# Kernel optimization log

Hardware: AMD Instinct MI355X
Metric: run time of the kernel (lower is better)

## Reference

```python
import jax, jax.numpy as jnp
import numpy as np

NUM_EMBEDDINGS = 256
EMBEDDING_DIM = 8


def setup_inputs() -> dict:
    key = jax.random.key(0)
    ks = jax.random.split(key, 8)
    B, D_in, H, D_out = 1024, 512, 2048, 512
    s = lambda fan: 1.0 / np.sqrt(fan)
    return {
        "x": jax.random.normal(ks[0], (B, D_in), dtype=jnp.float32),
        "emb_W": jax.random.normal(ks[1], (NUM_EMBEDDINGS, EMBEDDING_DIM), dtype=jnp.float32),
        "W_in": jax.random.normal(ks[2], (H, D_in), dtype=jnp.float32) * s(D_in),
        "b_in": jax.random.normal(ks[3], (H,), dtype=jnp.float32) * s(D_in),
        "W_h": jax.random.normal(ks[4], (H, H), dtype=jnp.float32) * s(H),
        "b_h": jax.random.normal(ks[5], (H,), dtype=jnp.float32) * s(H),
        "W_out": jax.random.normal(ks[6], (D_out, H), dtype=jnp.float32) * s(H),
        "b_out": jax.random.normal(ks[7], (D_out,), dtype=jnp.float32) * s(H),
    }


def reference(x, emb_W, W_in, b_in, W_h, b_h, W_out, b_out):
    B, D_in = x.shape
    flat = x.reshape(-1)  # [B*D_in], row-major flatten == torch .flatten()
    # power-feature expansion: powers 1..embedding_dim stacked on axis 1
    exps = jnp.arange(1, EMBEDDING_DIM + 1, dtype=x.dtype)
    x_res = flat[:, None] ** exps[None, :]  # [B*D_in, E]
    # get_ind: NOTE source uses sum(flat_x) (not sum of squares) -- faithful
    sm = jnp.sum(x_res, axis=1, keepdims=True)              # [N,1]
    emb = jnp.sum(emb_W * emb_W, axis=1)[None, :]           # [1,K]
    dist = sm + emb - 2.0 * (x_res @ emb_W.T)               # [N,K]
    ind = jnp.argmin(dist, axis=1)                          # [N] int
    # q = ind.view_as(x.T).T : reshape to [D_in, B] then transpose
    q = ind.reshape(D_in, B).T.astype(x.dtype)              # [B, D_in]
    # straight-through: forward value q, gradient flows to x
    q = x + jax.lax.stop_gradient(q - x)
    relu = jax.nn.relu
    h = relu(q @ W_in.T + b_in)      # d_in
    for _ in range(4):               # shared d_h applied 4 times
        h = relu(h @ W_h.T + b_h)
    f = relu(h @ W_out.T + b_out)    # d_out
    q_latent_loss = jnp.float32(0.0)  # eval mode
    return (f, q_latent_loss)
```

## Files before the change

### kernel.cpp

```cpp
#include <hip/hip_runtime.h>
#include <hip/hip_bf16.h>
#include <math.h>


#define B_ROWS 1024
#define D_IN   512
#define HDIM   2048
#define NTOT   (B_ROWS * D_IN)
#define NCODE  256
#define EDIM   8

typedef __attribute__((ext_vector_type(8))) short bf16x8;
typedef __attribute__((ext_vector_type(4))) float f32x4;

__device__ inline void gload_lds16(const void* g, void* l) {
    __builtin_amdgcn_global_load_lds(
        (const __attribute__((address_space(1))) void*)g,
        (__attribute__((address_space(3))) void*)l, 16, 0, 0);
}

__device__ inline ushort bf16_hi_bits(float v, float* hi_f) {
    __hip_bfloat16 h = __float2bfloat16(v);
    *hi_f = __bfloat162float(h);
    ushort u; __builtin_memcpy(&u, &h, 2); return u;
}
__device__ inline ushort bf16_bits(float v) {
    __hip_bfloat16 h = __float2bfloat16(v);
    ushort u; __builtin_memcpy(&u, &h, 2); return u;
}

__global__ __launch_bounds__(256) void fused_pre(
    const float* __restrict__ x, const float* __restrict__ embW,
    const float* __restrict__ Wi, const float* __restrict__ Wh,
    ushort* __restrict__ qhi,
    ushort* __restrict__ wihi, ushort* __restrict__ wilo,
    ushort* __restrict__ whhi, ushort* __restrict__ whlo,
    float* __restrict__ loss_out)
{
    __shared__ float sWE[NCODE][12];
    const int tid = threadIdx.x;

    if (blockIdx.x >= 1024) {
        const int sidx = blockIdx.x - 1024;
        #pragma unroll
        for (int s = 0; s < 4; ++s) {
            const int g = sidx * 1024 + s * 256 + tid;
            const float* src; ushort* hi; ushort* lo; int j;
            if (g < 262144) { src = Wi; hi = wihi; lo = wilo; j = g; }
            else            { src = Wh; hi = whhi; lo = whlo; j = g - 262144; }
            float4 v = reinterpret_cast<const float4*>(src)[j];
            float f[4] = {v.x, v.y, v.z, v.w};
            ushort hh[4], ll[4];
            #pragma unroll
            for (int c = 0; c < 4; ++c) {
                float hf;
                hh[c] = bf16_hi_bits(f[c], &hf);
                ll[c] = bf16_bits(f[c] - hf);
            }
            ushort4 h4 = {hh[0], hh[1], hh[2], hh[3]};
            ushort4 l4 = {ll[0], ll[1], ll[2], ll[3]};
            reinterpret_cast<ushort4*>(hi)[j] = h4;
            reinterpret_cast<ushort4*>(lo)[j] = l4;
        }
        return;
    }

    {
        const float4 a4 = *reinterpret_cast<const float4*>(&embW[tid * EDIM]);
        const float4 b4 = *reinterpret_cast<const float4*>(&embW[tid * EDIM + 4]);
        float s0 = __fmul_rn(a4.x, a4.x), s1 = __fmul_rn(a4.y, a4.y);
        float s2 = __fmul_rn(a4.z, a4.z), s3 = __fmul_rn(a4.w, a4.w);
        float s4 = __fmul_rn(b4.x, b4.x), s5 = __fmul_rn(b4.y, b4.y);
        float s6 = __fmul_rn(b4.z, b4.z), s7 = __fmul_rn(b4.w, b4.w);
        float a = __fadd_rn(__fadd_rn(s0, s1), __fadd_rn(s2, s3));
        float b = __fadd_rn(__fadd_rn(s4, s5), __fadd_rn(s6, s7));
        sWE[tid][0] = a4.x; sWE[tid][1] = a4.y; sWE[tid][2] = a4.z; sWE[tid][3] = a4.w;
        sWE[tid][4] = b4.x; sWE[tid][5] = b4.y; sWE[tid][6] = b4.z; sWE[tid][7] = b4.w;
        sWE[tid][8] = __fadd_rn(a, b);
    }
    __syncthreads();

    const int nbase = blockIdx.x * 512 + tid;

    float p2[2][EDIM], sm[2];
    #pragma unroll
    for (int j = 0; j < 2; ++j) {
        const float v = x[nbase + j * 256];
        float p[EDIM];
        #pragma unroll
        for (int e = 0; e < EDIM; ++e)
            p[e] = powf(v, (float)(e + 1));
        float a = __fadd_rn(__fadd_rn(p[0], p[1]), __fadd_rn(p[2], p[3]));
        float b = __fadd_rn(__fadd_rn(p[4], p[5]), __fadd_rn(p[6], p[7]));
        sm[j] = __fadd_rn(a, b);
        #pragma unroll
        for (int e = 0; e < EDIM; ++e)
            p2[j][e] = 2.0f * p[e];
    }

    float best[2] = {INFINITY, INFINITY};
    int   bi[2]   = {0, 0};
    for (int k = 0; k < NCODE; ++k) {
        const float4 w0 = *reinterpret_cast<const float4*>(&sWE[k][0]);
        const float4 w1 = *reinterpret_cast<const float4*>(&sWE[k][4]);
        const float  Ek = sWE[k][8];
        #pragma unroll
        for (int j = 0; j < 2; ++j) {
            float dot = 0.f;
            dot = fmaf(p2[j][0], w0.x, dot); dot = fmaf(p2[j][1], w0.y, dot);
            dot = fmaf(p2[j][2], w0.z, dot); dot = fmaf(p2[j][3], w0.w, dot);
            dot = fmaf(p2[j][4], w1.x, dot); dot = fmaf(p2[j][5], w1.y, dot);
            dot = fmaf(p2[j][6], w1.z, dot); dot = fmaf(p2[j][7], w1.w, dot);
            float d = __fsub_rn(__fadd_rn(sm[j], Ek), dot);
            if (d < best[j]) { best[j] = d; bi[j] = k; }
        }
    }

    #pragma unroll
    for (int j = 0; j < 2; ++j) {
        const int n  = nbase + j * 256;
        const int bo = n & (B_ROWS - 1);
        const int dd = n >> 10;
        qhi[bo * D_IN + dd] = bf16_bits((float)bi[j]);
    }
    if (blockIdx.x == 0 && tid == 0) loss_out[0] = 0.0f;
}

__global__ __launch_bounds__(256) void wo_split(
    const float* __restrict__ Wo, ushort* __restrict__ hi, ushort* __restrict__ lo)
{
    const int tid = threadIdx.x;
    #pragma unroll
    for (int s = 0; s < 4; ++s) {
        const int j = blockIdx.x * 1024 + s * 256 + tid;
        float4 v = reinterpret_cast<const float4*>(Wo)[j];
        float f[4] = {v.x, v.y, v.z, v.w};
        ushort hh[4], ll[4];
        #pragma unroll
        for (int c = 0; c < 4; ++c) {
            float hf;
            hh[c] = bf16_hi_bits(f[c], &hf);
            ll[c] = bf16_bits(f[c] - hf);
        }
        ushort4 h4 = {hh[0], hh[1], hh[2], hh[3]};
        ushort4 l4 = {ll[0], ll[1], ll[2], ll[3]};
        reinterpret_cast<ushort4*>(hi)[j] = h4;
        reinterpret_cast<ushort4*>(lo)[j] = l4;
    }
}

template<bool ALO, bool PARTIAL>
__global__ __launch_bounds__(256) void gemm_split(
    const ushort* __restrict__ Ahi, const ushort* __restrict__ Alo,
    const ushort* __restrict__ Whi, const ushort* __restrict__ Wlo,
    const float* __restrict__ bias,
    ushort* __restrict__ Ohi, ushort* __restrict__ Olo,
    float* __restrict__ OF, int N, int K, int klen)
{
    constexpr int BUF = 49152;
    constexpr int OFF_AH = 0, OFF_AL = 8192, OFF_BH = 16384;
    __shared__ char lds[2 * BUF];

    const int tid = threadIdx.x, lane = tid & 63, wid = tid >> 6;

    const int gy = gridDim.y;
    const int nwg = gridDim.x * gy;
    int lin = blockIdx.x * gy + blockIdx.y;
    int q   = nwg >> 3;
    int sw  = (lin & 7) * q + (lin >> 3);
    int bx  = sw / gy, by2 = sw % gy;
    const int bm   = (by2 & 15) << 6;
    const int kz   = by2 >> 4;
    const int kbeg = kz * klen;
    const int bn   = bx << 7;

    const int wm = (wid >> 1) << 5;
    const int wn = (wid & 1) << 6;

    constexpr int NSEGW = ALO ? 12 : 10;
    const ushort* gp[NSEGW];
    uint ldsoff[NSEGW];
    #pragma unroll
    for (int i = 0; i < NSEGW; ++i) {
        int s = wid + i * 4;
        const ushort* pl; int row0, base, sip;
        if (ALO) {
            if (s < 8)       { pl = Ahi; row0 = bm; base = OFF_AH;         sip = s; }
            else if (s < 16) { pl = Alo; row0 = bm; base = OFF_AL;         sip = s - 8; }
            else if (s < 32) { pl = Whi; row0 = bn; base = OFF_BH;         sip = s - 16; }
            else             { pl = Wlo; row0 = bn; base = OFF_BH + 16384; sip = s - 32; }
        } else {
            if (s < 8)       { pl = Ahi; row0 = bm; base = OFF_AH;         sip = s; }
            else if (s < 24) { pl = Whi; row0 = bn; base = OFF_BH;         sip = s - 8; }
            else             { pl = Wlo; row0 = bn; base = OFF_BH + 16384; sip = s - 24; }
        }
        int r  = sip * 8 + (lane >> 3);
        int ch = (lane & 7) ^ (r & 7);
        gp[i]     = pl + (size_t)(row0 + r) * K + kbeg + ch * 8;
        ldsoff[i] = base + sip * 1024;
    }

    uint aoff[2][2], boff[4][2];
    #pragma unroll
    for (int f = 0; f < 2; ++f) {
        int ar = wm + f * 16 + (lane & 15);
        #pragma unroll
        for (int s = 0; s < 2; ++s) {
            int ch = (s * 4 + (lane >> 4)) ^ (ar & 7);
            aoff[f][s] = OFF_AH + ar * 128 + ch * 16;
        }
    }
    #pragma unroll
    for (int f = 0; f < 4; ++f) {
        int br = wn + f * 16 + (lane & 15);
        #pragma unroll
        for (int s = 0; s < 2; ++s) {
            int ch = (s * 4 + (lane >> 4)) ^ (br & 7);
            boff[f][s] = OFF_BH + br * 128 + ch * 16;
        }
    }

    auto stage = [&](int kt, int b) {
        #pragma unroll
        for (int i = 0; i < NSEGW; ++i)
            gload_lds16(gp[i] + kt * 64, lds + b * BUF + ldsoff[i]);
    };

    f32x4 acc[2][4] = {};
    const int NT = klen >> 6;

    stage(0, 0);
    __syncthreads();

    for (int t = 0; t < NT; ++t) {
        const int cur = t & 1;
        if (t + 1 < NT) stage(t + 1, cur ^ 1);

        const char* lb = lds + cur * BUF;
        bf16x8 aH[2][2], aL[2][2], bH[2][4], bL[2][4];
        #pragma unroll
        for (int s = 0; s < 2; ++s) {
            #pragma unroll
            for (int f = 0; f < 2; ++f) {
                aH[s][f] = *(const bf16x8*)(lb + aoff[f][s]);
                if constexpr (ALO) aL[s][f] = *(const bf16x8*)(lb + aoff[f][s] + 8192);
            }
            #pragma unroll
            for (int f = 0; f < 4; ++f) {
                bH[s][f] = *(const bf16x8*)(lb + boff[f][s]);
                bL[s][f] = *(const bf16x8*)(lb + boff[f][s] + 16384);
            }
        }
        #pragma unroll
        for (int s = 0; s < 2; ++s) {
            #pragma unroll
            for (int fm = 0; fm < 2; ++fm)
                #pragma unroll
                for (int fn = 0; fn < 4; ++fn)
                    acc[fm][fn] = __builtin_amdgcn_mfma_f32_16x16x32_bf16(
                        aH[s][fm], bH[s][fn], acc[fm][fn], 0, 0, 0);
            #pragma unroll
            for (int fm = 0; fm < 2; ++fm)
                #pragma unroll
                for (int fn = 0; fn < 4; ++fn)
                    acc[fm][fn] = __builtin_amdgcn_mfma_f32_16x16x32_bf16(
                        aH[s][fm], bL[s][fn], acc[fm][fn], 0, 0, 0);
            if constexpr (ALO) {
                #pragma unroll
                for (int fm = 0; fm < 2; ++fm)
                    #pragma unroll
                    for (int fn = 0; fn < 4; ++fn)
                        acc[fm][fn] = __builtin_amdgcn_mfma_f32_16x16x32_bf16(
                            aL[s][fm], bH[s][fn], acc[fm][fn], 0, 0, 0);
            }
        }
        __syncthreads();
    }

    #pragma unroll
    for (int fm = 0; fm < 2; ++fm) {
        #pragma unroll
        for (int fn = 0; fn < 4; ++fn) {
            const int col = bn + wn + fn * 16 + (lane & 15);
            const int rb  = bm + wm + fm * 16 + ((lane >> 4) << 2);
            if constexpr (PARTIAL) {
                #pragma unroll
                for (int r = 0; r < 4; ++r)
                    OF[(size_t)(kz * B_ROWS + rb + r) * N + col] = acc[fm][fn][r];
            } else {
                const float bc = bias[col];
                #pragma unroll
                for (int r = 0; r < 4; ++r) {
                    float v = acc[fm][fn][r] + bc;
                    v = v > 0.f ? v : 0.f;
                    float hf;
                    ushort hb = bf16_hi_bits(v, &hf);
                    Ohi[(size_t)(rb + r) * N + col] = hb;
                    Olo[(size_t)(rb + r) * N + col] = bf16_bits(v - hf);
                }
            }
        }
    }
}

__global__ __launch_bounds__(256) void gemm_mid(
    const ushort* __restrict__ Ahi, const ushort* __restrict__ Alo,
    const ushort* __restrict__ Bhi, const ushort* __restrict__ Blo,
    float* __restrict__ OF, int N, int Kfull, int klen)
{
    constexpr int BUF = 65536;
    constexpr int OFF_A[2] = {0, 16384};
    constexpr int OFF_B[2] = {32768, 49152};
    __shared__ char lds[2 * BUF];

    const int tid = threadIdx.x, lane = tid & 63, wid = tid >> 6;

    const int gy = gridDim.y;
    const int nwg = gridDim.x * gy;
    int lin = blockIdx.x * gy + blockIdx.y;
    int q   = nwg >> 3;
    int sw  = (lin & 7) * q + (lin >> 3);
    int bx  = sw / gy, by2 = sw % gy;
    const int bm   = (by2 & 7) << 7;
    const int kz   = by2 >> 3;
    const int kbeg = kz * klen;
    const int bn   = bx << 7;

    const int wm = (wid >> 1) << 6;
    const int wn = (wid & 1) << 6;

    const int ch0 = (lane & 7) ^ (lane >> 3);
    const size_t kstep8 = (size_t)Kfull * 8;
    const ushort* gpb[4];
    uint lob[4];
    {
        const ushort* pls[4] = {Ahi, Alo, Bhi, Blo};
        const int row0s[4]   = {bm, bm, bn, bn};
        const uint bases[4]  = {OFF_A[0], OFF_A[1], OFF_B[0], OFF_B[1]};
        #pragma unroll
        for (int p = 0; p < 4; ++p) {
            gpb[p] = pls[p] + (size_t)(row0s[p] + wid * 32 + (lane >> 3)) * Kfull
                     + kbeg + ch0 * 8;
            lob[p] = bases[p] + wid * 4096;
        }
    }

    uint aoff[4][2], boff[4][2];
    #pragma unroll
    for (int f = 0; f < 4; ++f) {
        #pragma unroll
        for (int ks = 0; ks < 2; ++ks) {
            int ch = (ks * 4 + (lane >> 4)) ^ (lane & 7);
            aoff[f][ks] = OFF_A[0] + (wm + f * 16 + (lane & 15)) * 128 + ch * 16;
            boff[f][ks] = OFF_B[0] + (wn + f * 16 + (lane & 15)) * 128 + ch * 16;
        }
    }

    auto stage = [&](int kt, int b) {
        #pragma unroll
        for (int p = 0; p < 4; ++p)
            #pragma unroll
            for (int i = 0; i < 4; ++i)
                gload_lds16(gpb[p] + i * kstep8 + kt * 64,
                            lds + b * BUF + lob[p] + i * 1024);
    };

    f32x4 acc[4][4] = {};
    const int NT = klen >> 6;

    stage(0, 0);
    __syncthreads();

    for (int t = 0; t < NT; ++t) {
        const int cur = t & 1;
        if (t + 1 < NT) stage(t + 1, cur ^ 1);

        const char* lb = lds + cur * BUF;
        #pragma unroll
        for (int ks = 0; ks < 2; ++ks) {
            bf16x8 aH[4], aL[4], bH[4], bL[4];
            #pragma unroll
            for (int f = 0; f < 4; ++f) {
                aH[f] = *(const bf16x8*)(lb + aoff[f][ks]);
                aL[f] = *(const bf16x8*)(lb + aoff[f][ks] + 16384);
                bH[f] = *(const bf16x8*)(lb + boff[f][ks]);
                bL[f] = *(const bf16x8*)(lb + boff[f][ks] + 16384);
            }
            #pragma unroll
            for (int fm = 0; fm < 4; ++fm)
                #pragma unroll
                for (int fn = 0; fn < 4; ++fn)
                    acc[fm][fn] = __builtin_amdgcn_mfma_f32_16x16x32_bf16(
                        aH[fm], bH[fn], acc[fm][fn], 0, 0, 0);
            #pragma unroll
            for (int fm = 0; fm < 4; ++fm)
                #pragma unroll
                for (int fn = 0; fn < 4; ++fn)
                    acc[fm][fn] = __builtin_amdgcn_mfma_f32_16x16x32_bf16(
                        aH[fm], bL[fn], acc[fm][fn], 0, 0, 0);
            #pragma unroll
            for (int fm = 0; fm < 4; ++fm)
                #pragma unroll
                for (int fn = 0; fn < 4; ++fn)
                    acc[fm][fn] = __builtin_amdgcn_mfma_f32_16x16x32_bf16(
                        aL[fm], bH[fn], acc[fm][fn], 0, 0, 0);
        }
        __syncthreads();
    }

    #pragma unroll
    for (int fm = 0; fm < 4; ++fm) {
        #pragma unroll
        for (int fn = 0; fn < 4; ++fn) {
            const int col = bn + wn + fn * 16 + (lane & 15);
            const int rb  = bm + wm + fm * 16 + ((lane >> 4) << 2);
            #pragma unroll
            for (int r = 0; r < 4; ++r)
                OF[(size_t)(kz * B_ROWS + rb + r) * N + col] = acc[fm][fn][r];
        }
    }
}

__global__ __launch_bounds__(256) void combine_mid(
    const float* __restrict__ part, const float* __restrict__ bias,
    ushort* __restrict__ hi, ushort* __restrict__ lo)
{
    const int i = blockIdx.x * 256 + threadIdx.x;
    const float4* p = (const float4*)part;
    float4 a = p[i], b = p[i + 524288];
    float4 bb = ((const float4*)bias)[i & 511];
    float f[4] = {a.x + b.x + bb.x, a.y + b.y + bb.y,
                  a.z + b.z + bb.z, a.w + b.w + bb.w};
    ushort hh[4], ll[4];
    #pragma unroll
    for (int c = 0; c < 4; ++c) {
        float v = f[c] > 0.f ? f[c] : 0.f;
        float hf;
        hh[c] = bf16_hi_bits(v, &hf);
        ll[c] = bf16_bits(v - hf);
    }
    ushort4 h4 = {hh[0], hh[1], hh[2], hh[3]};
    ushort4 l4 = {ll[0], ll[1], ll[2], ll[3]};
    reinterpret_cast<ushort4*>(hi)[i] = h4;
    reinterpret_cast<ushort4*>(lo)[i] = l4;
}

__global__ __launch_bounds__(256) void combine_relu(
    const float* __restrict__ part, const float* __restrict__ bias,
    float* __restrict__ out)
{
    const int i = blockIdx.x * 256 + threadIdx.x;
    const float4* p = (const float4*)part;
    float4 a = p[i], b = p[i + 131072], c = p[i + 262144], d = p[i + 393216];
    float4 bb = ((const float4*)bias)[i & 127];
    float4 o;
    o.x = a.x + b.x + c.x + d.x + bb.x;
    o.y = a.y + b.y + c.y + d.y + bb.y;
    o.z = a.z + b.z + c.z + d.z + bb.z;
    o.w = a.w + b.w + c.w + d.w + bb.w;
    o.x = o.x > 0.f ? o.x : 0.f;
    o.y = o.y > 0.f ? o.y : 0.f;
    o.z = o.z > 0.f ? o.z : 0.f;
    o.w = o.w > 0.f ? o.w : 0.f;
    reinterpret_cast<float4*>(out)[i] = o;
}

extern "C" void kernel_launch(void* const* d_in, const int* in_sizes, int n_in,
                              void* d_out, int out_size, void* d_ws, size_t ws_size,
                              hipStream_t stream)
{
    const float* x     = (const float*)d_in[0];
    const float* emb_W = (const float*)d_in[1];
    const float* W_in  = (const float*)d_in[2];
    const float* b_in  = (const float*)d_in[3];
    const float* W_h   = (const float*)d_in[4];
    const float* b_h   = (const float*)d_in[5];
    const float* W_out = (const float*)d_in[6];
    const float* b_out = (const float*)d_in[7];
    float* out = (float*)d_out;

    char* w = (char*)d_ws;
    const size_t MB = 1 << 20;
    ushort* qhi    = (ushort*)(w);
    ushort* wihi   = (ushort*)(w + 1*MB);
    ushort* wilo   = (ushort*)(w + 3*MB);
    float*  midpar = (float*)(w);
    ushort* wohi   = (ushort*)(w);
    ushort* wolo   = (ushort*)(w + 2*MB);
    float*  l6par  = (float*)(w + 4*MB);
    ushort* hhi    = (ushort*)(w + 16*MB);
    ushort* hlo    = (ushort*)(w + 20*MB);
    ushort* whhi   = (ushort*)(w + 24*MB);
    ushort* whlo   = (ushort*)(w + 32*MB);

    fused_pre<<<2304, 256, 0, stream>>>(x, emb_W, W_in, W_h,
                                        qhi, wihi, wilo, whhi, whlo, out + NTOT);

    gemm_split<false, false><<<dim3(16, 16), 256, 0, stream>>>(
        qhi, nullptr, wihi, wilo, b_in, hhi, hlo, nullptr, HDIM, D_IN, D_IN);

    for (int l = 0; l < 4; ++l) {
        gemm_mid<<<dim3(16, 16), 256, 0, stream>>>(
            hhi, hlo, whhi, whlo, midpar, HDIM, HDIM, 1024);
        combine_mid<<<2048, 256, 0, stream>>>(midpar, b_h, hhi, hlo);
    }

    wo_split<<<256, 256, 0, stream>>>(W_out, wohi, wolo);

    gemm_mid<<<dim3(4, 32), 256, 0, stream>>>(
        hhi, hlo, wohi, wolo, l6par, D_IN, HDIM, D_IN);

    combine_relu<<<512, 256, 0, stream>>>(l6par, b_out, out);
}
```

Measured before the change: 217.7 us.

## Triple-buffer mid GEMM with BK=32 and read codebook from global

The mid-layer split-K GEMM moves from a double-buffered 64-wide K tile to a triple-buffered 32-wide K tile. Each wave loads one operand plane, with a new XOR swizzle, and the loop waits on vmcnt plus a single barrier so loads run two stages ahead of the MFMAs. The aim is to hide global-to-LDS latency and cut LDS footprint per stage. The quantizer kernel now keeps only the codebook norms in shared memory and reads codebook vectors straight from global (cached), which trades LDS traffic for scalar/global loads.

```diff
diff --git a/kernel.cpp b/kernel.cpp
--- a/kernel.cpp
+++ b/kernel.cpp
@@ -37,7 +37,7 @@
     ushort* __restrict__ whhi, ushort* __restrict__ whlo,
     float* __restrict__ loss_out)
 {
-    __shared__ float sWE[NCODE][12];
+    __shared__ float sE[NCODE];
     const int tid = threadIdx.x;
 
     if (blockIdx.x >= 1024) {
@@ -74,9 +74,7 @@
         float s6 = __fmul_rn(b4.z, b4.z), s7 = __fmul_rn(b4.w, b4.w);
         float a = __fadd_rn(__fadd_rn(s0, s1), __fadd_rn(s2, s3));
         float b = __fadd_rn(__fadd_rn(s4, s5), __fadd_rn(s6, s7));
-        sWE[tid][0] = a4.x; sWE[tid][1] = a4.y; sWE[tid][2] = a4.z; sWE[tid][3] = a4.w;
-        sWE[tid][4] = b4.x; sWE[tid][5] = b4.y; sWE[tid][6] = b4.z; sWE[tid][7] = b4.w;
-        sWE[tid][8] = __fadd_rn(a, b);
+        sE[tid] = __fadd_rn(a, b);
     }
     __syncthreads();
 
@@ -100,10 +98,11 @@
 
     float best[2] = {INFINITY, INFINITY};
     int   bi[2]   = {0, 0};
+    #pragma unroll 2
     for (int k = 0; k < NCODE; ++k) {
-        const float4 w0 = *reinterpret_cast<const float4*>(&sWE[k][0]);
-        const float4 w1 = *reinterpret_cast<const float4*>(&sWE[k][4]);
-        const float  Ek = sWE[k][8];
+        const float4 w0 = *reinterpret_cast<const float4*>(&embW[k * EDIM]);
+        const float4 w1 = *reinterpret_cast<const float4*>(&embW[k * EDIM + 4]);
+        const float  Ek = sE[k];
         #pragma unroll
         for (int j = 0; j < 2; ++j) {
             float dot = 0.f;
@@ -308,10 +307,8 @@
     const ushort* __restrict__ Bhi, const ushort* __restrict__ Blo,
     float* __restrict__ OF, int N, int Kfull, int klen)
 {
-    constexpr int BUF = 65536;
-    constexpr int OFF_A[2] = {0, 16384};
-    constexpr int OFF_B[2] = {32768, 49152};
-    __shared__ char lds[2 * BUF];
+    constexpr int BUFSZ = 32768;
+    __shared__ char lds[3 * BUFSZ];
 
     const int tid = threadIdx.x, lane = tid & 63, wid = tid >> 6;
 
@@ -329,83 +326,78 @@
     const int wm = (wid >> 1) << 6;
     const int wn = (wid & 1) << 6;
 
-    const int ch0 = (lane & 7) ^ (lane >> 3);
-    const size_t kstep8 = (size_t)Kfull * 8;
-    const ushort* gpb[4];
-    uint lob[4];
-    {
-        const ushort* pls[4] = {Ahi, Alo, Bhi, Blo};
-        const int row0s[4]   = {bm, bm, bn, bn};
-        const uint bases[4]  = {OFF_A[0], OFF_A[1], OFF_B[0], OFF_B[1]};
-        #pragma unroll
-        for (int p = 0; p < 4; ++p) {
-            gpb[p] = pls[p] + (size_t)(row0s[p] + wid * 32 + (lane >> 3)) * Kfull
-                     + kbeg + ch0 * 8;
-            lob[p] = bases[p] + wid * 4096;
-        }
-    }
-
-    uint aoff[4][2], boff[4][2];
+    const ushort* plp = (wid == 0) ? Ahi : (wid == 1) ? Alo
+                       : (wid == 2) ? Bhi : Blo;
+    const int  prow0 = (wid < 2) ? bm : bn;
+    const uint pbase = (uint)wid * 8192;
+    const int  r_l   = lane >> 2;
+    const int  chs   = (lane & 3) ^ ((r_l >> 1) & 3);
+    const ushort* gp[8];
+    uint lo_[8];
+    #pragma unroll
+    for (int i = 0; i < 8; ++i) {
+        gp[i]  = plp + (size_t)(prow0 + i * 16 + r_l) * Kfull + kbeg + chs * 8;
+        lo_[i] = pbase + i * 1024 + (uint)lane * 16;
+    }
+
+    uint aoff[4], boff[4];
     #pragma unroll
     for (int f = 0; f < 4; ++f) {
-        #pragma unroll
-        for (int ks = 0; ks < 2; ++ks) {
-            int ch = (ks * 4 + (lane >> 4)) ^ (lane & 7);
-            aoff[f][ks] = OFF_A[0] + (wm + f * 16 + (lane & 15)) * 128 + ch * 16;
-            boff[f][ks] = OFF_B[0] + (wn + f * 16 + (lane & 15)) * 128 + ch * 16;
-        }
+        const int ar = wm + f * 16 + (lane & 15);
+        aoff[f] = (uint)(ar * 64 + ((((lane >> 4)) ^ ((ar >> 1) & 3)) << 4));
+        const int br = wn + f * 16 + (lane & 15);
+        boff[f] = (uint)(16384 + br * 64 + ((((lane >> 4)) ^ ((br >> 1) & 3)) << 4));
     }
 
     auto stage = [&](int kt, int b) {
         #pragma unroll
-        for (int p = 0; p < 4; ++p)
-            #pragma unroll
-            for (int i = 0; i < 4; ++i)
-                gload_lds16(gpb[p] + i * kstep8 + kt * 64,
-                            lds + b * BUF + lob[p] + i * 1024);
+        for (int i = 0; i < 8; ++i)
+            gload_lds16(gp[i] + kt * 32, lds + b * BUFSZ + (lo_[i] - (uint)lane * 16));
     };
 
     f32x4 acc[4][4] = {};
-    const int NT = klen >> 6;
+    const int NT = klen >> 5;
 
     stage(0, 0);
-    __syncthreads();
-
+    stage(1, 1);
+
+    int cb = 0, sb = 2;
     for (int t = 0; t < NT; ++t) {
-        const int cur = t & 1;
-        if (t + 1 < NT) stage(t + 1, cur ^ 1);
-
-        const char* lb = lds + cur * BUF;
-        #pragma unroll
-        for (int ks = 0; ks < 2; ++ks) {
-            bf16x8 aH[4], aL[4], bH[4], bL[4];
-            #pragma unroll
-            for (int f = 0; f < 4; ++f) {
-                aH[f] = *(const bf16x8*)(lb + aoff[f][ks]);
-                aL[f] = *(const bf16x8*)(lb + aoff[f][ks] + 16384);
-                bH[f] = *(const bf16x8*)(lb + boff[f][ks]);
-                bL[f] = *(const bf16x8*)(lb + boff[f][ks] + 16384);
-            }
-            #pragma unroll
-            for (int fm = 0; fm < 4; ++fm)
-                #pragma unroll
-                for (int fn = 0; fn < 4; ++fn)
-                    acc[fm][fn] = __builtin_amdgcn_mfma_f32_16x16x32_bf16(
-                        aH[fm], bH[fn], acc[fm][fn], 0, 0, 0);
-            #pragma unroll
-            for (int fm = 0; fm < 4; ++fm)
-                #pragma unroll
-                for (int fn = 0; fn < 4; ++fn)
-                    acc[fm][fn] = __builtin_amdgcn_mfma_f32_16x16x32_bf16(
-                        aH[fm], bL[fn], acc[fm][fn], 0, 0, 0);
-            #pragma unroll
-            for (int fm = 0; fm < 4; ++fm)
-                #pragma unroll
-                for (int fn = 0; fn < 4; ++fn)
-                    acc[fm][fn] = __builtin_amdgcn_mfma_f32_16x16x32_bf16(
-                        aL[fm], bH[fn], acc[fm][fn], 0, 0, 0);
-        }
-        __syncthreads();
+        if (t + 1 < NT) { asm volatile("s_waitcnt vmcnt(8)" ::: "memory"); }
+        else            { asm volatile("s_waitcnt vmcnt(0)" ::: "memory"); }
+        __builtin_amdgcn_s_barrier();
+        if (t + 2 < NT) stage(t + 2, sb);
+
+        const char* lb = lds + cb * BUFSZ;
+        bf16x8 aH[4], aL[4], bH[4], bL[4];
+        #pragma unroll
+        for (int f = 0; f < 4; ++f) {
+            aH[f] = *(const bf16x8*)(lb + aoff[f]);
+            aL[f] = *(const bf16x8*)(lb + aoff[f] + 8192);
+            bH[f] = *(const bf16x8*)(lb + boff[f]);
+            bL[f] = *(const bf16x8*)(lb + boff[f] + 8192);
+        }
+        #pragma unroll
+        for (int fm = 0; fm < 4; ++fm)
+            #pragma unroll
+            for (int fn = 0; fn < 4; ++fn)
+                acc[fm][fn] = __builtin_amdgcn_mfma_f32_16x16x32_bf16(
+                    aH[fm], bH[fn], acc[fm][fn], 0, 0, 0);
+        #pragma unroll
+        for (int fm = 0; fm < 4; ++fm)
+            #pragma unroll
+            for (int fn = 0; fn < 4; ++fn)
+                acc[fm][fn] = __builtin_amdgcn_mfma_f32_16x16x32_bf16(
+                    aH[fm], bL[fn], acc[fm][fn], 0, 0, 0);
+        #pragma unroll
+        for (int fm = 0; fm < 4; ++fm)
+            #pragma unroll
+            for (int fn = 0; fn < 4; ++fn)
+                acc[fm][fn] = __builtin_amdgcn_mfma_f32_16x16x32_bf16(
+                    aL[fm], bH[fn], acc[fm][fn], 0, 0, 0);
+
+        cb = (cb == 2) ? 0 : cb + 1;
+        sb = (sb == 2) ? 0 : sb + 1;
     }
 
     #pragma unroll
```

New measurement: 237.1 us. 8.9% more time.

## Shrink gemm_mid tile to 128x64 with 32-wide K steps for higher occupancy

Applied to the files above, without the earlier changes.

Reworks the split-bf16 GEMM kernel to use 128x64 output tiles and 32-element K steps. This cuts LDS use to 48KB, so launch bounds can ask for three blocks per CU and the grid doubles to fill more of the GPU. The final output layer now uses an 8-way K split with its partial buffer moved, and combine_relu sums eight partials instead of four. The trade-off is less data reuse per tile, more global loads per FLOP, and more partial-sum traffic in the last layer.

```diff
diff --git a/kernel.cpp b/kernel.cpp
--- a/kernel.cpp
+++ b/kernel.cpp
@@ -303,15 +303,13 @@
     }
 }
 
-__global__ __launch_bounds__(256) void gemm_mid(
+__global__ __launch_bounds__(256, 3) void gemm_mid(
     const ushort* __restrict__ Ahi, const ushort* __restrict__ Alo,
     const ushort* __restrict__ Bhi, const ushort* __restrict__ Blo,
     float* __restrict__ OF, int N, int Kfull, int klen)
 {
-    constexpr int BUF = 65536;
-    constexpr int OFF_A[2] = {0, 16384};
-    constexpr int OFF_B[2] = {32768, 49152};
-    __shared__ char lds[2 * BUF];
+    constexpr int BUFSZ = 24576;
+    __shared__ char lds[2 * BUFSZ];
 
     const int tid = threadIdx.x, lane = tid & 63, wid = tid >> 6;
 
@@ -324,49 +322,47 @@
     const int bm   = (by2 & 7) << 7;
     const int kz   = by2 >> 3;
     const int kbeg = kz * klen;
-    const int bn   = bx << 7;
+    const int bn   = bx << 6;
 
     const int wm = (wid >> 1) << 6;
-    const int wn = (wid & 1) << 6;
-
-    const int ch0 = (lane & 7) ^ (lane >> 3);
-    const size_t kstep8 = (size_t)Kfull * 8;
-    const ushort* gpb[4];
-    uint lob[4];
-    {
-        const ushort* pls[4] = {Ahi, Alo, Bhi, Blo};
-        const int row0s[4]   = {bm, bm, bn, bn};
-        const uint bases[4]  = {OFF_A[0], OFF_A[1], OFF_B[0], OFF_B[1]};
-        #pragma unroll
-        for (int p = 0; p < 4; ++p) {
-            gpb[p] = pls[p] + (size_t)(row0s[p] + wid * 32 + (lane >> 3)) * Kfull
-                     + kbeg + ch0 * 8;
-            lob[p] = bases[p] + wid * 4096;
-        }
-    }
-
-    uint aoff[4][2], boff[4][2];
+    const int wn = (wid & 1) << 5;
+
+    const int r_l = lane >> 2;
+    const int chs = (lane & 3) ^ ((r_l >> 1) & 3);
+    const ushort* gp[6];
+    uint ldsoff[6];
+    #pragma unroll
+    for (int i = 0; i < 6; ++i) {
+        const int s = wid + i * 4;
+        const ushort* pl; int row0; uint base;
+        if (s < 8)       { pl = Ahi; row0 = bm + s * 16;        base = (uint)s * 1024; }
+        else if (s < 16) { pl = Alo; row0 = bm + (s - 8) * 16;  base = 8192  + (uint)(s - 8)  * 1024; }
+        else if (s < 20) { pl = Bhi; row0 = bn + (s - 16) * 16; base = 16384 + (uint)(s - 16) * 1024; }
+        else             { pl = Blo; row0 = bn + (s - 20) * 16; base = 20480 + (uint)(s - 20) * 1024; }
+        gp[i]     = pl + (size_t)(row0 + r_l) * Kfull + kbeg + chs * 8;
+        ldsoff[i] = base;
+    }
+
+    uint aoff[4], boff[2];
     #pragma unroll
     for (int f = 0; f < 4; ++f) {
-        #pragma unroll
-        for (int ks = 0; ks < 2; ++ks) {
-            int ch = (ks * 4 + (lane >> 4)) ^ (lane & 7);
-            aoff[f][ks] = OFF_A[0] + (wm + f * 16 + (lane & 15)) * 128 + ch * 16;
-            boff[f][ks] = OFF_B[0] + (wn + f * 16 + (lane & 15)) * 128 + ch * 16;
-        }
+        const int ar = wm + f * 16 + (lane & 15);
+        aoff[f] = (uint)(ar * 64 + ((((lane >> 4)) ^ ((ar >> 1) & 3)) << 4));
+    }
+    #pragma unroll
+    for (int f = 0; f < 2; ++f) {
+        const int br = wn + f * 16 + (lane & 15);
+        boff[f] = (uint)(16384 + br * 64 + ((((lane >> 4)) ^ ((br >> 1) & 3)) << 4));
     }
 
     auto stage = [&](int kt, int b) {
         #pragma unroll
-        for (int p = 0; p < 4; ++p)
-            #pragma unroll
-            for (int i = 0; i < 4; ++i)
-                gload_lds16(gpb[p] + i * kstep8 + kt * 64,
-                            lds + b * BUF + lob[p] + i * 1024);
+        for (int i = 0; i < 6; ++i)
+            gload_lds16(gp[i] + kt * 32, lds + b * BUFSZ + ldsoff[i]);
     };
 
-    f32x4 acc[4][4] = {};
-    const int NT = klen >> 6;
+    f32x4 acc[4][2] = {};
+    const int NT = klen >> 5;
 
     stage(0, 0);
     __syncthreads();
@@ -375,43 +371,43 @@
         const int cur = t & 1;
         if (t + 1 < NT) stage(t + 1, cur ^ 1);
 
-        const char* lb = lds + cur * BUF;
-        #pragma unroll
-        for (int ks = 0; ks < 2; ++ks) {
-            bf16x8 aH[4], aL[4], bH[4], bL[4];
-            #pragma unroll
-            for (int f = 0; f < 4; ++f) {
-                aH[f] = *(const bf16x8*)(lb + aoff[f][ks]);
-                aL[f] = *(const bf16x8*)(lb + aoff[f][ks] + 16384);
-                bH[f] = *(const bf16x8*)(lb + boff[f][ks]);
-                bL[f] = *(const bf16x8*)(lb + boff[f][ks] + 16384);
-            }
-            #pragma unroll
-            for (int fm = 0; fm < 4; ++fm)
-                #pragma unroll
-                for (int fn = 0; fn < 4; ++fn)
-                    acc[fm][fn] = __builtin_amdgcn_mfma_f32_16x16x32_bf16(
-                        aH[fm], bH[fn], acc[fm][fn], 0, 0, 0);
-            #pragma unroll
-            for (int fm = 0; fm < 4; ++fm)
-                #pragma unroll
-                for (int fn = 0; fn < 4; ++fn)
-                    acc[fm][fn] = __builtin_amdgcn_mfma_f32_16x16x32_bf16(
-                        aH[fm], bL[fn], acc[fm][fn], 0, 0, 0);
-            #pragma unroll
-            for (int fm = 0; fm < 4; ++fm)
-                #pragma unroll
-                for (int fn = 0; fn < 4; ++fn)
-                    acc[fm][fn] = __builtin_amdgcn_mfma_f32_16x16x32_bf16(
-                        aL[fm], bH[fn], acc[fm][fn], 0, 0, 0);
-        }
+        const char* lb = lds + cur * BUFSZ;
+        bf16x8 aH[4], aL[4], bH[2], bL[2];
+        #pragma unroll
+        for (int f = 0; f < 4; ++f) {
+            aH[f] = *(const bf16x8*)(lb + aoff[f]);
+            aL[f] = *(const bf16x8*)(lb + aoff[f] + 8192);
+        }
+        #pragma unroll
+        for (int f = 0; f < 2; ++f) {
+            bH[f] = *(const bf16x8*)(lb + boff[f]);
+            bL[f] = *(const bf16x8*)(lb + boff[f] + 4096);
+        }
+        #pragma unroll
+        for (int fm = 0; fm < 4; ++fm)
+            #pragma unroll
+            for (int fn = 0; fn < 2; ++fn)
+                acc[fm][fn] = __builtin_amdgcn_mfma_f32_16x16x32_bf16(
+                    aH[fm], bH[fn], acc[fm][fn], 0, 0, 0);
+        #pragma unroll
+        for (int fm = 0; fm < 4; ++fm)
+            #pragma unroll
+            for (int fn = 0; fn < 2; ++fn)
+                acc[fm][fn] = __builtin_amdgcn_mfma_f32_16x16x32_bf16(
+                    aH[fm], bL[fn], acc[fm][fn], 0, 0, 0);
+        #pragma unroll
+        for (int fm = 0; fm < 4; ++fm)
+            #pragma unroll
+            for (int fn = 0; fn < 2; ++fn)
+                acc[fm][fn] = __builtin_amdgcn_mfma_f32_16x16x32_bf16(
+                    aL[fm], bH[fn], acc[fm][fn], 0, 0, 0);
         __syncthreads();
     }
 
     #pragma unroll
     for (int fm = 0; fm < 4; ++fm) {
         #pragma unroll
-        for (int fn = 0; fn < 4; ++fn) {
+        for (int fn = 0; fn < 2; ++fn) {
             const int col = bn + wn + fn * 16 + (lane & 15);
             const int rb  = bm + wm + fm * 16 + ((lane >> 4) << 2);
             #pragma unroll
@@ -451,17 +447,18 @@
 {
     const int i = blockIdx.x * 256 + threadIdx.x;
     const float4* p = (const float4*)part;
-    float4 a = p[i], b = p[i + 131072], c = p[i + 262144], d = p[i + 393216];
     float4 bb = ((const float4*)bias)[i & 127];
+    float ox = bb.x, oy = bb.y, oz = bb.z, ow = bb.w;
+    #pragma unroll
+    for (int z = 0; z < 8; ++z) {
+        float4 a = p[i + z * 131072];
+        ox += a.x; oy += a.y; oz += a.z; ow += a.w;
+    }
     float4 o;
-    o.x = a.x + b.x + c.x + d.x + bb.x;
-    o.y = a.y + b.y + c.y + d.y + bb.y;
-    o.z = a.z + b.z + c.z + d.z + bb.z;
-    o.w = a.w + b.w + c.w + d.w + bb.w;
-    o.x = o.x > 0.f ? o.x : 0.f;
-    o.y = o.y > 0.f ? o.y : 0.f;
-    o.z = o.z > 0.f ? o.z : 0.f;
-    o.w = o.w > 0.f ? o.w : 0.f;
+    o.x = ox > 0.f ? ox : 0.f;
+    o.y = oy > 0.f ? oy : 0.f;
+    o.z = oz > 0.f ? oz : 0.f;
+    o.w = ow > 0.f ? ow : 0.f;
     reinterpret_cast<float4*>(out)[i] = o;
 }
 
@@ -487,11 +484,11 @@
     float*  midpar = (float*)(w);
     ushort* wohi   = (ushort*)(w);
     ushort* wolo   = (ushort*)(w + 2*MB);
-    float*  l6par  = (float*)(w + 4*MB);
     ushort* hhi    = (ushort*)(w + 16*MB);
     ushort* hlo    = (ushort*)(w + 20*MB);
     ushort* whhi   = (ushort*)(w + 24*MB);
     ushort* whlo   = (ushort*)(w + 32*MB);
+    float*  l6par  = (float*)(w + 24*MB);
 
     fused_pre<<<2304, 256, 0, stream>>>(x, emb_W, W_in, W_h,
                                         qhi, wihi, wilo, whhi, whlo, out + NTOT);
@@ -500,15 +497,15 @@
         qhi, nullptr, wihi, wilo, b_in, hhi, hlo, nullptr, HDIM, D_IN, D_IN);
 
     for (int l = 0; l < 4; ++l) {
-        gemm_mid<<<dim3(16, 16), 256, 0, stream>>>(
+        gemm_mid<<<dim3(32, 16), 256, 0, stream>>>(
             hhi, hlo, whhi, whlo, midpar, HDIM, HDIM, 1024);
         combine_mid<<<2048, 256, 0, stream>>>(midpar, b_h, hhi, hlo);
     }
 
     wo_split<<<256, 256, 0, stream>>>(W_out, wohi, wolo);
 
-    gemm_mid<<<dim3(4, 32), 256, 0, stream>>>(
-        hhi, hlo, wohi, wolo, l6par, D_IN, HDIM, D_IN);
+    gemm_mid<<<dim3(8, 64), 256, 0, stream>>>(
+        hhi, hlo, wohi, wolo, l6par, D_IN, HDIM, 256);
 
     combine_relu<<<512, 256, 0, stream>>>(l6par, b_out, out);
 }
```

Result: slower. 236.8 us (+8.7%).
